# Kernel tuning notes

Hardware: AMD Instinct MI355X
Metric: run time of the kernel (lower is better)

The kernel has to match this reference:

```python
import jax, jax.numpy as jnp
import numpy as np

D = 2048  # dims
T = 8192  # sequence length


def _layernorm(x, g, b):
    m = jnp.mean(x, axis=-1, keepdims=True)
    v = jnp.mean(jnp.square(x - m), axis=-1, keepdims=True)
    return (x - m) * jax.lax.rsqrt(v + 1e-5) * g + b


def _lerp(a, b, t):
    # torch.lerp(a, b, t) = a + t*(b-a)
    return a + t * (b - a)


def _wkv(k, v, time_first, time_decay):
    """RWKV power-decay attention (numerically stable scan).
    k, v: [T, D]. w = -exp(time_decay) is the per-channel log-decay."""
    u = time_first
    w = -jnp.exp(time_decay)

    def step(carry, kv):
        aa, bb, pp = carry  # running num, den, max-exponent, each [D]
        kt, vt = kv
        ww = u + kt
        p = jnp.maximum(pp, ww)
        e1 = jnp.exp(pp - p)
        e2 = jnp.exp(ww - p)
        out = (e1 * aa + e2 * vt) / (e1 * bb + e2)
        ww2 = pp + w
        p2 = jnp.maximum(ww2, kt)
        e1 = jnp.exp(ww2 - p2)
        e2 = jnp.exp(kt - p2)
        return (e1 * aa + e2 * vt, e1 * bb + e2, p2), out

    init = (jnp.zeros((D,), k.dtype), jnp.zeros((D,), k.dtype),
            jnp.full((D,), -1e38, k.dtype))
    _, out = jax.lax.scan(step, init, (k, v))
    return out  # [T, D]


def setup_inputs() -> dict:
    key = jax.random.key(0)
    ks = iter(jax.random.split(key, 40))
    s = 1.0 / np.sqrt(D)
    inp = {"x": jax.random.normal(next(ks), (T, D), jnp.float32)}
    for name in ["attk", "attv", "attr", "atto", "ffnk", "ffnv", "ffnr"]:
        inp[name + "_w"] = jax.random.normal(next(ks), (D, D), jnp.float32) * s
        inp[name + "_b"] = jax.random.normal(next(ks), (D,), jnp.float32) * 0.02
    inp["ln1_g"] = jnp.ones((D,), jnp.float32)
    inp["ln1_b"] = jnp.zeros((D,), jnp.float32)
    inp["ln2_g"] = jnp.ones((D,), jnp.float32)
    inp["ln2_b"] = jnp.zeros((D,), jnp.float32)
    for name in ["attmixk", "attmixv", "attmixr", "ffnmixk", "ffnmixr"]:
        inp[name] = jax.random.uniform(next(ks), (D,), jnp.float32)
    inp["time_first"] = jax.random.normal(next(ks), (D,), jnp.float32) * 0.1
    inp["time_decay"] = jax.random.normal(next(ks), (D,), jnp.float32) * 0.1
    return inp


def reference(x, attk_w, attk_b, attv_w, attv_b, attr_w, attr_b, atto_w, atto_b,
              ffnk_w, ffnk_b, ffnv_w, ffnv_b, ffnr_w, ffnr_b,
              ln1_g, ln1_b, ln2_g, ln2_b,
              attmixk, attmixv, attmixr, ffnmixk, ffnmixr,
              time_first, time_decay):
    # --- time-mix (attention) branch ---
    xy = _layernorm(x, ln1_g, ln1_b)
    tc = jnp.roll(xy, 1, axis=0)  # token shift
    k = _lerp(tc, xy, attmixk) @ attk_w.T + attk_b
    v = _lerp(tc, xy, attmixv) @ attv_w.T + attv_b
    r = jax.nn.sigmoid(_lerp(tc, xy, attmixr) @ attr_w.T + attr_b)
    wkv = _wkv(k, v, time_first, time_decay) * r
    rz = x + wkv @ atto_w.T + atto_b
    # --- channel-mix (FFN) branch ---
    ddd = _layernorm(rz, ln2_g, ln2_b)
    rc = jnp.roll(ddd, 1, axis=0)
    rf = jax.nn.sigmoid(_lerp(rc, ddd, ffnmixr) @ ffnr_w.T + ffnr_b)
    kf = jax.nn.relu(_lerp(rc, ddd, ffnmixk) @ ffnk_w.T + ffnk_b)
    rvm = jnp.square(kf) @ ffnv_w.T + ffnv_b
    return rvm * rf + rz
```

## Files before the change

### kernel.cpp

```cpp
#include <hip/hip_runtime.h>
#include <cstdint>
#include <cstddef>


#define SEQ 8192
#define DIM 2048
#define NCH 128
#define CL  64

typedef unsigned short u16;
typedef __attribute__((ext_vector_type(8))) short bf16x8;
typedef __attribute__((ext_vector_type(4))) float f32x4;

__device__ __forceinline__ u16 f2bf(float f) {
  unsigned x = __float_as_uint(f);
  x += 0x7fffu + ((x >> 16) & 1u);
  return (u16)(x >> 16);
}
__device__ __forceinline__ float bf2f(u16 h) {
  return __uint_as_float((unsigned)h << 16);
}

__global__ void __launch_bounds__(256) convert_weights(
    const float* w0, const float* w1, const float* w2, const float* w3,
    const float* w4, const float* w5, const float* w6, u16* dst)
{
  const float* s;
  switch (blockIdx.y) {
    case 0: s = w0; break; case 1: s = w1; break; case 2: s = w2; break;
    case 3: s = w3; break; case 4: s = w4; break; case 5: s = w5; break;
    default: s = w6; break;
  }
  size_t i = ((size_t)blockIdx.x * 256 + threadIdx.x) * 4;
  float4 f = *(const float4*)(s + i);
  *(ushort4*)(dst + (size_t)blockIdx.y * DIM * DIM + i) =
      make_ushort4(f2bf(f.x), f2bf(f.y), f2bf(f.z), f2bf(f.w));
}

__device__ __forceinline__ void store_mix8(u16* dst, const float* mix,
                                           const float* yc, const float* yp)
{
  float4 ma = *(const float4*)(mix);
  float4 mb = *(const float4*)(mix + 4);
  float mv[8] = {ma.x, ma.y, ma.z, ma.w, mb.x, mb.y, mb.z, mb.w};
  u16 uu[8];
  #pragma unroll
  for (int j = 0; j < 8; ++j)
    uu[j] = f2bf(yp[j] + mv[j] * (yc[j] - yp[j]));
  *(ushort4*)dst       = make_ushort4(uu[0], uu[1], uu[2], uu[3]);
  *(ushort4*)(dst + 4) = make_ushort4(uu[4], uu[5], uu[6], uu[7]);
}

template<int NOUT>
__global__ void __launch_bounds__(256) ln_mix_kernel(
    const float* __restrict__ X, const float* __restrict__ gw, const float* __restrict__ bw,
    const float* __restrict__ mix0, const float* __restrict__ mix1, const float* __restrict__ mix2,
    u16* __restrict__ o0, u16* __restrict__ o1, u16* __restrict__ o2)
{
  const int t  = blockIdx.x;
  const int tp = (t == 0) ? (SEQ - 1) : (t - 1);
  const int tid = threadIdx.x, lane = tid & 63, wid = tid >> 6;
  const int base = tid * 8;
  const float* xc = X + (size_t)t  * DIM + base;
  const float* xp = X + (size_t)tp * DIM + base;
  float4 ca = *(const float4*)xc, cb2 = *(const float4*)(xc + 4);
  float4 pa = *(const float4*)xp, pb2 = *(const float4*)(xp + 4);
  float cv[8] = {ca.x, ca.y, ca.z, ca.w, cb2.x, cb2.y, cb2.z, cb2.w};
  float pv[8] = {pa.x, pa.y, pa.z, pa.w, pb2.x, pb2.y, pb2.z, pb2.w};
  float4 s = {0.f, 0.f, 0.f, 0.f};
  #pragma unroll
  for (int j = 0; j < 8; ++j) {
    s.x += cv[j]; s.y += cv[j] * cv[j];
    s.z += pv[j]; s.w += pv[j] * pv[j];
  }
  #pragma unroll
  for (int off = 32; off > 0; off >>= 1) {
    s.x += __shfl_down(s.x, off);
    s.y += __shfl_down(s.y, off);
    s.z += __shfl_down(s.z, off);
    s.w += __shfl_down(s.w, off);
  }
  __shared__ float4 wred[4];
  if (lane == 0) wred[wid] = s;
  __syncthreads();
  float4 tt;
  tt.x = wred[0].x + wred[1].x + wred[2].x + wred[3].x;
  tt.y = wred[0].y + wred[1].y + wred[2].y + wred[3].y;
  tt.z = wred[0].z + wred[1].z + wred[2].z + wred[3].z;
  tt.w = wred[0].w + wred[1].w + wred[2].w + wred[3].w;
  constexpr float inv = 1.0f / DIM;
  const float mc = tt.x * inv, vc = tt.y * inv - mc * mc;
  const float rc = 1.0f / sqrtf(vc + 1e-5f);
  const float mp = tt.z * inv, vp = tt.w * inv - mp * mp;
  const float rp = 1.0f / sqrtf(vp + 1e-5f);
  float4 ga = *(const float4*)(gw + base), gb = *(const float4*)(gw + base + 4);
  float4 ba = *(const float4*)(bw + base), bb = *(const float4*)(bw + base + 4);
  float gv[8] = {ga.x, ga.y, ga.z, ga.w, gb.x, gb.y, gb.z, gb.w};
  float bv[8] = {ba.x, ba.y, ba.z, ba.w, bb.x, bb.y, bb.z, bb.w};
  float yc[8], yp[8];
  #pragma unroll
  for (int j = 0; j < 8; ++j) {
    yc[j] = (cv[j] - mc) * rc * gv[j] + bv[j];
    yp[j] = (pv[j] - mp) * rp * gv[j] + bv[j];
  }
  store_mix8(o0 + (size_t)t * DIM + base, mix0 + base, yc, yp);
  store_mix8(o1 + (size_t)t * DIM + base, mix1 + base, yc, yp);
  if constexpr (NOUT == 3)
    store_mix8(o2 + (size_t)t * DIM + base, mix2 + base, yc, yp);
}

template<int EPI>
__global__ void __launch_bounds__(512, 2) gemm_bt(
    const u16* __restrict__ A, const u16* __restrict__ B,
    const float* __restrict__ bias,
    const float* __restrict__ exf, const u16* __restrict__ exb,
    float* __restrict__ Cf, u16* __restrict__ Cb)
{
  constexpr int BK = 32;
  constexpr int NT = DIM / BK;
  __shared__ u16 As[4][256 * BK];
  __shared__ u16 Bs[4][256 * BK];
  const int tid  = threadIdx.x;
  const int lane = tid & 63;
  const int wid  = tid >> 6;
  const int wr   = wid >> 2;
  const int wc   = wid & 3;
  const int bid = blockIdx.x;
  const int nb  = (bid & 7) * 32 + (bid >> 3);
  const int tm  = (nb >> 3) * 256;
  const int tn  = (nb & 7) * 256;
  const int frow = lane & 15;
  const int fkc  = lane >> 4;

  f32x4 acc[8][4] = {};

#define STAGE(b, kt)                                                            \
  {                                                                             \
    const int k0 = (kt) * BK;                                                   \
    _Pragma("unroll")                                                           \
    for (int j = 0; j < 2; ++j) {                                               \
      const int p   = (j * 512 + tid) * 16;                                     \
      const int q   = p ^ (((p >> 7) & 3) << 4);                                \
      const int row = q >> 6;                                                   \
      const int ce  = (q & 63) >> 1;                                            \
      __builtin_amdgcn_global_load_lds(                                         \
          (const __attribute__((address_space(1))) void*)                       \
              (A + (size_t)(tm + row) * DIM + k0 + ce),                         \
          (__attribute__((address_space(3))) void*)((char*)&As[b][0] + p),      \
          16, 0, 0);                                                            \
    }                                                                           \
    _Pragma("unroll")                                                           \
    for (int j = 0; j < 2; ++j) {                                               \
      const int p   = (j * 512 + tid) * 16;                                     \
      const int q   = p ^ (((p >> 7) & 3) << 4);                                \
      const int row = q >> 6;                                                   \
      const int ce  = (q & 63) >> 1;                                            \
      __builtin_amdgcn_global_load_lds(                                         \
          (const __attribute__((address_space(1))) void*)                       \
              (B + (size_t)(tn + row) * DIM + k0 + ce),                         \
          (__attribute__((address_space(3))) void*)((char*)&Bs[b][0] + p),      \
          16, 0, 0);                                                            \
    }                                                                           \
  }

#define COMPUTE(b)                                                              \
  {                                                                             \
    bf16x8 af[8], bfr[4];                                                       \
    _Pragma("unroll")                                                           \
    for (int m = 0; m < 8; ++m) {                                               \
      const int row = wr * 128 + m * 16 + frow;                                 \
      const int off = row * 64 + ((fkc ^ ((row >> 1) & 3)) * 16);               \
      af[m] = *(const bf16x8*)((const char*)&As[b][0] + off);                   \
    }                                                                           \
    _Pragma("unroll")                                                           \
    for (int n = 0; n < 4; ++n) {                                               \
      const int row = wc * 64 + n * 16 + frow;                                  \
      const int off = row * 64 + ((fkc ^ ((row >> 1) & 3)) * 16);               \
      bfr[n] = *(const bf16x8*)((const char*)&Bs[b][0] + off);                  \
    }                                                                           \
    __builtin_amdgcn_s_setprio(1);                                              \
    _Pragma("unroll")                                                           \
    for (int m = 0; m < 8; ++m)                                                 \
      _Pragma("unroll")                                                         \
      for (int n = 0; n < 4; ++n)                                               \
        acc[m][n] = __builtin_amdgcn_mfma_f32_16x16x32_bf16(af[m], bfr[n],      \
                                                            acc[m][n], 0, 0, 0);\
    __builtin_amdgcn_s_setprio(0);                                              \
  }

  STAGE(0, 0); STAGE(1, 1); STAGE(2, 2);
  #pragma unroll 1
  for (int t = 0; t < NT - 2; ++t) {
    asm volatile("s_waitcnt vmcnt(8)" ::: "memory");
    __builtin_amdgcn_s_barrier();
    __builtin_amdgcn_sched_barrier(0);
    if (t < NT - 3) STAGE((t + 3) & 3, t + 3);
    COMPUTE(t & 3);
  }
  asm volatile("s_waitcnt vmcnt(4)" ::: "memory");
  __builtin_amdgcn_s_barrier();
  __builtin_amdgcn_sched_barrier(0);
  COMPUTE((NT - 2) & 3);
  asm volatile("s_waitcnt vmcnt(0)" ::: "memory");
  __builtin_amdgcn_s_barrier();
  __builtin_amdgcn_sched_barrier(0);
  COMPUTE((NT - 1) & 3);
#undef STAGE
#undef COMPUTE

  #pragma unroll
  for (int n = 0; n < 4; ++n) {
    const int cn = tn + wc * 64 + n * 16 + frow;
    const float bv = bias[cn];
    #pragma unroll
    for (int m = 0; m < 8; ++m) {
      const int r0 = tm + wr * 128 + m * 16 + (lane >> 4) * 4;
      #pragma unroll
      for (int i = 0; i < 4; ++i) {
        const size_t idx = (size_t)(r0 + i) * DIM + cn;
        float val = acc[m][n][i] + bv;
        if constexpr (EPI == 0)      { Cb[idx] = f2bf(val); }
        else if constexpr (EPI == 1) { Cb[idx] = f2bf(1.0f / (1.0f + __expf(-val))); }
        else if constexpr (EPI == 2) { Cf[idx] = val + exf[idx]; }
        else if constexpr (EPI == 3) { float r = fmaxf(val, 0.0f); Cb[idx] = f2bf(r * r); }
        else                         { Cf[idx] = val * bf2f(exb[idx]) + exf[idx]; }
      }
    }
  }
}

__global__ void __launch_bounds__(256) wkv_phase1(
    const u16* __restrict__ k, const u16* __restrict__ v,
    const float* __restrict__ tdec,
    float* __restrict__ Sa, float* __restrict__ Sb, float* __restrict__ Sp)
{
  const int d = blockIdx.y * 256 + threadIdx.x;
  const int c = blockIdx.x;
  const float w = -__expf(tdec[d]);
  float aa = 0.f, bb = 0.f, pp = -1e38f;
  const int t0 = c * CL;
  for (int t = t0; t < t0 + CL; ++t) {
    const size_t idx = (size_t)t * DIM + d;
    const float kk = bf2f(k[idx]), vv = bf2f(v[idx]);
    const float ww2 = pp + w;
    const float p2 = fmaxf(ww2, kk);
    const float e1 = __expf(ww2 - p2), e2 = __expf(kk - p2);
    aa = e1 * aa + e2 * vv;
    bb = e1 * bb + e2;
    pp = p2;
  }
  Sa[(size_t)c * DIM + d] = aa;
  Sb[(size_t)c * DIM + d] = bb;
  Sp[(size_t)c * DIM + d] = pp;
}

__global__ void __launch_bounds__(256) wkv_phase2(
    const float* __restrict__ Sa, const float* __restrict__ Sb, const float* __restrict__ Sp,
    const float* __restrict__ tdec,
    float* __restrict__ Pa, float* __restrict__ Pb, float* __restrict__ Pp)
{
  const int d = blockIdx.x * 256 + threadIdx.x;
  const float w = -__expf(tdec[d]);
  const float Lw = (float)CL * w;
  float aa = 0.f, bb = 0.f, pp = -1e38f;
  for (int c = 0; c < NCH; ++c) {
    const size_t idx = (size_t)c * DIM + d;
    Pa[idx] = aa; Pb[idx] = bb; Pp[idx] = pp;
    const float dp = pp + Lw;
    const float sa = Sa[idx], sb = Sb[idx], sp = Sp[idx];
    const float p = fmaxf(dp, sp);
    const float e1 = __expf(dp - p), e2 = __expf(sp - p);
    aa = e1 * aa + e2 * sa;
    bb = e1 * bb + e2 * sb;
    pp = p;
  }
}

__global__ void __launch_bounds__(256) wkv_phase3(
    const u16* __restrict__ k, const u16* __restrict__ v, const u16* __restrict__ r,
    const float* __restrict__ Pa, const float* __restrict__ Pb, const float* __restrict__ Pp,
    const float* __restrict__ tfirst, const float* __restrict__ tdec,
    u16* __restrict__ outb)
{
  const int d = blockIdx.y * 256 + threadIdx.x;
  const int c = blockIdx.x;
  const float u = tfirst[d];
  const float w = -__expf(tdec[d]);
  const size_t sidx = (size_t)c * DIM + d;
  float aa = Pa[sidx], bb = Pb[sidx], pp = Pp[sidx];
  const int t0 = c * CL;
  for (int t = t0; t < t0 + CL; ++t) {
    const size_t idx = (size_t)t * DIM + d;
    const float kk = bf2f(k[idx]), vv = bf2f(v[idx]);
    const float ww = u + kk;
    const float p = fmaxf(pp, ww);
    float e1 = __expf(pp - p), e2 = __expf(ww - p);
    const float out = (e1 * aa + e2 * vv) / (e1 * bb + e2);
    outb[idx] = f2bf(out * bf2f(r[idx]));
    const float ww2 = pp + w;
    const float p2 = fmaxf(ww2, kk);
    e1 = __expf(ww2 - p2); e2 = __expf(kk - p2);
    aa = e1 * aa + e2 * vv;
    bb = e1 * bb + e2;
    pp = p2;
  }
}

extern "C" void kernel_launch(void* const* d_in, const int* in_sizes, int n_in,
                              void* d_out, int out_size, void* d_ws, size_t ws_size,
                              hipStream_t stream)
{
  const float* x      = (const float*)d_in[0];
  const float* attk_w = (const float*)d_in[1];
  const float* attk_b = (const float*)d_in[2];
  const float* attv_w = (const float*)d_in[3];
  const float* attv_b = (const float*)d_in[4];
  const float* attr_w = (const float*)d_in[5];
  const float* attr_b = (const float*)d_in[6];
  const float* atto_w = (const float*)d_in[7];
  const float* atto_b = (const float*)d_in[8];
  const float* ffnk_w = (const float*)d_in[9];
  const float* ffnk_b = (const float*)d_in[10];
  const float* ffnv_w = (const float*)d_in[11];
  const float* ffnv_b = (const float*)d_in[12];
  const float* ffnr_w = (const float*)d_in[13];
  const float* ffnr_b = (const float*)d_in[14];
  const float* ln1_g  = (const float*)d_in[15];
  const float* ln1_b  = (const float*)d_in[16];
  const float* ln2_g  = (const float*)d_in[17];
  const float* ln2_b  = (const float*)d_in[18];
  const float* amixk  = (const float*)d_in[19];
  const float* amixv  = (const float*)d_in[20];
  const float* amixr  = (const float*)d_in[21];
  const float* fmixk  = (const float*)d_in[22];
  const float* fmixr  = (const float*)d_in[23];
  const float* tfirst = (const float*)d_in[24];
  const float* tdecay = (const float*)d_in[25];
  float* out = (float*)d_out;

  const size_t WE = (size_t)DIM * DIM;
  const size_t SD = (size_t)SEQ * DIM;
  u16* Wbf = (u16*)d_ws;
  u16* xk  = Wbf + 7 * WE;
  u16* xv  = xk + SD;
  u16* xr  = xv + SD;
  u16* kb  = xr + SD;
  u16* vb  = kb + SD;
  u16* rb  = vb + SD;
  float* Sa = (float*)(rb + SD);
  float* Sb = Sa + (size_t)NCH * DIM;
  float* Sp = Sb + (size_t)NCH * DIM;
  float* Pa = Sp + (size_t)NCH * DIM;
  float* Pb = Pa + (size_t)NCH * DIM;
  float* Pp = Pb + (size_t)NCH * DIM;
  u16*   wkvr = xk;
  float* rz   = (float*)xv;
  u16*   xkf  = kb;
  u16*   xrf  = vb;
  u16*   rf   = rb;
  u16*   kf2  = xk;

  const dim3 gg(256);
  const dim3 gwkv(NCH, DIM / 256);

  convert_weights<<<dim3(DIM * DIM / 1024, 7), 256, 0, stream>>>(
      attk_w, attv_w, attr_w, atto_w, ffnk_w, ffnv_w, ffnr_w, Wbf);

  ln_mix_kernel<3><<<SEQ, 256, 0, stream>>>(x, ln1_g, ln1_b, amixk, amixv, amixr, xk, xv, xr);
  gemm_bt<0><<<gg, 512, 0, stream>>>(xk, Wbf + 0 * WE, attk_b, nullptr, nullptr, nullptr, kb);
  gemm_bt<0><<<gg, 512, 0, stream>>>(xv, Wbf + 1 * WE, attv_b, nullptr, nullptr, nullptr, vb);
  gemm_bt<1><<<gg, 512, 0, stream>>>(xr, Wbf + 2 * WE, attr_b, nullptr, nullptr, nullptr, rb);
  wkv_phase1<<<gwkv, 256, 0, stream>>>(kb, vb, tdecay, Sa, Sb, Sp);
  wkv_phase2<<<DIM / 256, 256, 0, stream>>>(Sa, Sb, Sp, tdecay, Pa, Pb, Pp);
  wkv_phase3<<<gwkv, 256, 0, stream>>>(kb, vb, rb, Pa, Pb, Pp, tfirst, tdecay, wkvr);
  gemm_bt<2><<<gg, 512, 0, stream>>>(wkvr, Wbf + 3 * WE, atto_b, x, nullptr, rz, nullptr);

  ln_mix_kernel<2><<<SEQ, 256, 0, stream>>>(rz, ln2_g, ln2_b, fmixk, fmixr, nullptr, xkf, xrf, nullptr);
  gemm_bt<1><<<gg, 512, 0, stream>>>(xrf, Wbf + 6 * WE, ffnr_b, nullptr, nullptr, nullptr, rf);
  gemm_bt<3><<<gg, 512, 0, stream>>>(xkf, Wbf + 4 * WE, ffnk_b, nullptr, nullptr, nullptr, kf2);
  gemm_bt<4><<<gg, 512, 0, stream>>>(kf2, Wbf + 5 * WE, ffnv_b, rz, rf, out, nullptr);
}
```

Baseline: 1.124 ms.

## Restructure GEMM mainloop into 8-wave ping-pong schedule with BK=64 quadrant stages

Rewrites the bf16 GEMM main loop to use a K tile of 64 with double-buffered LDS split into 128-row halves. Each tile is processed in four sub-blocks (A lo/hi by B lo/hi). Global-to-LDS loads for the next half-tiles are interleaved between these sub-blocks, and barriers and setprio are arranged in a hipBLASLt-style ping-pong. The aim is to overlap LDS reads, global loads and MFMA more finely and to halve the number of K iterations. The cost is many more barriers per iteration, plus the risk that the hand-placed waitcnt accounting races or under-hides latency.

Measured after the change: 1.148 ms. +2.2%, slower.

```diff
diff --git a/kernel.cpp b/kernel.cpp
--- a/kernel.cpp
+++ b/kernel.cpp
@@ -116,10 +116,11 @@
     const float* __restrict__ exf, const u16* __restrict__ exb,
     float* __restrict__ Cf, u16* __restrict__ Cb)
 {
-  constexpr int BK = 32;
-  constexpr int NT = DIM / BK;
-  __shared__ u16 As[4][256 * BK];
-  __shared__ u16 Bs[4][256 * BK];
+  constexpr int BK  = 64;
+  constexpr int NKT = DIM / BK;
+  constexpr int NIT = NKT / 2;
+  __shared__ u16 As[2][2][128 * 64];
+  __shared__ u16 Bs[2][2][128 * 64];
   const int tid  = threadIdx.x;
   const int lane = tid & 63;
   const int wid  = tid >> 6;
@@ -133,80 +134,135 @@
   const int fkc  = lane >> 4;
 
   f32x4 acc[8][4] = {};
-
-#define STAGE(b, kt)                                                            \
-  {                                                                             \
-    const int k0 = (kt) * BK;                                                   \
-    _Pragma("unroll")                                                           \
-    for (int j = 0; j < 2; ++j) {                                               \
-      const int p   = (j * 512 + tid) * 16;                                     \
-      const int q   = p ^ (((p >> 7) & 3) << 4);                                \
-      const int row = q >> 6;                                                   \
-      const int ce  = (q & 63) >> 1;                                            \
-      __builtin_amdgcn_global_load_lds(                                         \
-          (const __attribute__((address_space(1))) void*)                       \
-              (A + (size_t)(tm + row) * DIM + k0 + ce),                         \
-          (__attribute__((address_space(3))) void*)((char*)&As[b][0] + p),      \
-          16, 0, 0);                                                            \
-    }                                                                           \
-    _Pragma("unroll")                                                           \
-    for (int j = 0; j < 2; ++j) {                                               \
-      const int p   = (j * 512 + tid) * 16;                                     \
-      const int q   = p ^ (((p >> 7) & 3) << 4);                                \
-      const int row = q >> 6;                                                   \
-      const int ce  = (q & 63) >> 1;                                            \
-      __builtin_amdgcn_global_load_lds(                                         \
-          (const __attribute__((address_space(1))) void*)                       \
-              (B + (size_t)(tn + row) * DIM + k0 + ce),                         \
-          (__attribute__((address_space(3))) void*)((char*)&Bs[b][0] + p),      \
-          16, 0, 0);                                                            \
-    }                                                                           \
-  }
-
-#define COMPUTE(b)                                                              \
-  {                                                                             \
-    bf16x8 af[8], bfr[4];                                                       \
-    _Pragma("unroll")                                                           \
-    for (int m = 0; m < 8; ++m) {                                               \
-      const int row = wr * 128 + m * 16 + frow;                                 \
-      const int off = row * 64 + ((fkc ^ ((row >> 1) & 3)) * 16);               \
-      af[m] = *(const bf16x8*)((const char*)&As[b][0] + off);                   \
-    }                                                                           \
-    _Pragma("unroll")                                                           \
-    for (int n = 0; n < 4; ++n) {                                               \
-      const int row = wc * 64 + n * 16 + frow;                                  \
-      const int off = row * 64 + ((fkc ^ ((row >> 1) & 3)) * 16);               \
-      bfr[n] = *(const bf16x8*)((const char*)&Bs[b][0] + off);                  \
-    }                                                                           \
-    __builtin_amdgcn_s_setprio(1);                                              \
-    _Pragma("unroll")                                                           \
-    for (int m = 0; m < 8; ++m)                                                 \
-      _Pragma("unroll")                                                         \
-      for (int n = 0; n < 4; ++n)                                               \
-        acc[m][n] = __builtin_amdgcn_mfma_f32_16x16x32_bf16(af[m], bfr[n],      \
-                                                            acc[m][n], 0, 0, 0);\
-    __builtin_amdgcn_s_setprio(0);                                              \
-  }
-
-  STAGE(0, 0); STAGE(1, 1); STAGE(2, 2);
+  bf16x8 aLo[8], aHi[8], bLo[4], bHi[4];
+
+#define BAR  __builtin_amdgcn_s_barrier()
+#define LGK0 { asm volatile("s_waitcnt lgkmcnt(0)" ::: "memory");            \
+               __builtin_amdgcn_sched_barrier(0); }
+#define VMG(N) asm volatile("s_waitcnt vmcnt(" #N ")" ::: "memory")
+
+#define STGA(T, h)                                                            \
+  { _Pragma("unroll")                                                         \
+    for (int j = 0; j < 2; ++j) {                                             \
+      const int p  = (j * 512 + tid) * 16;                                    \
+      const int lr = p >> 7;                                                  \
+      const int cb = (p & 127) ^ ((lr & 7) << 4);                             \
+      __builtin_amdgcn_global_load_lds(                                       \
+        (const __attribute__((address_space(1))) void*)                       \
+            (A + (size_t)(tm + (h) * 128 + lr) * DIM + (T) * BK + (cb >> 1)), \
+        (__attribute__((address_space(3))) void*)((char*)&As[(T)&1][h][0]+p), \
+        16, 0, 0);                                                            \
+    } }
+#define STGB(T, h)                                                            \
+  { _Pragma("unroll")                                                         \
+    for (int j = 0; j < 2; ++j) {                                             \
+      const int p  = (j * 512 + tid) * 16;                                    \
+      const int lr = p >> 7;                                                  \
+      const int cb = (p & 127) ^ ((lr & 7) << 4);                             \
+      __builtin_amdgcn_global_load_lds(                                       \
+        (const __attribute__((address_space(1))) void*)                       \
+            (B + (size_t)(tn + (h) * 128 + lr) * DIM + (T) * BK + (cb >> 1)), \
+        (__attribute__((address_space(3))) void*)((char*)&Bs[(T)&1][h][0]+p), \
+        16, 0, 0);                                                            \
+    } }
+
+#define RDA(dst, db, mm, kk)                                                  \
+  { const int lr_ = (mm) * 16 + frow;                                         \
+    const int cb_ = (kk) * 64 + fkc * 16;                                     \
+    dst = *(const bf16x8*)((const char*)&As[db][wr][0]                        \
+          + lr_ * 128 + (cb_ ^ ((lr_ & 7) << 4))); }
+#define RDB(dst, db, nn, kk)                                                  \
+  { const int lr_ = (wc & 1) * 64 + (nn) * 16 + frow;                         \
+    const int cb_ = (kk) * 64 + fkc * 16;                                     \
+    dst = *(const bf16x8*)((const char*)&Bs[db][wc >> 1][0]                   \
+          + lr_ * 128 + (cb_ ^ ((lr_ & 7) << 4))); }
+
+#define MM(mb, nb_, AF, BF)                                                   \
+  do { __builtin_amdgcn_s_setprio(1);                                         \
+    _Pragma("unroll") for (int m = 0; m < 4; ++m)                             \
+    _Pragma("unroll") for (int n = 0; n < 2; ++n)                             \
+    _Pragma("unroll") for (int ks = 0; ks < 2; ++ks)                          \
+      acc[(mb)+m][(nb_)+n] = __builtin_amdgcn_mfma_f32_16x16x32_bf16(         \
+          (AF)[m*2+ks], (BF)[n*2+ks], acc[(mb)+m][(nb_)+n], 0, 0, 0);         \
+    __builtin_amdgcn_s_setprio(0); } while (0)
+
+#define ITER_BODY(i_, FIRST_, LAST_)                                          \
+  do {                                                                        \
+                                                                     \
+    _Pragma("unroll") for (int m = 0; m < 4; ++m)                             \
+      _Pragma("unroll") for (int ks = 0; ks < 2; ++ks)                        \
+        RDA(aLo[m*2+ks], 0, m, ks);                                           \
+    _Pragma("unroll") for (int n = 0; n < 2; ++n)                             \
+      _Pragma("unroll") for (int ks = 0; ks < 2; ++ks)                        \
+        RDB(bLo[n*2+ks], 0, n, ks);                                           \
+    if (!(FIRST_)) STGA(2*(i_)+1, 0);                                         \
+    BAR; LGK0; MM(0, 0, aLo, bLo); BAR;                                       \
+                                                                     \
+    _Pragma("unroll") for (int n = 0; n < 2; ++n)                             \
+      _Pragma("unroll") for (int ks = 0; ks < 2; ++ks)                        \
+        RDB(bHi[n*2+ks], 0, n + 2, ks);                                       \
+    if (!(FIRST_)) STGA(2*(i_)+1, 1);                                         \
+    BAR; LGK0; MM(0, 2, aLo, bHi); BAR;                                       \
+                                                                     \
+    _Pragma("unroll") for (int m = 0; m < 4; ++m)                             \
+      _Pragma("unroll") for (int ks = 0; ks < 2; ++ks)                        \
+        RDA(aHi[m*2+ks], 0, m + 4, ks);                                       \
+    if (!(LAST_)) STGB(2*(i_)+2, 0);                                          \
+    BAR; LGK0; MM(4, 0, aHi, bLo); BAR;                                       \
+                                               \
+    if (!(LAST_)) STGB(2*(i_)+2, 1);                                          \
+    BAR; MM(4, 2, aHi, bHi);                                                  \
+    if (LAST_) { VMG(0); } else { VMG(4); }                                   \
+    __builtin_amdgcn_sched_barrier(0);                                        \
+    BAR;                                                                      \
+                                                                     \
+    _Pragma("unroll") for (int m = 0; m < 4; ++m)                             \
+      _Pragma("unroll") for (int ks = 0; ks < 2; ++ks)                        \
+        RDA(aLo[m*2+ks], 1, m, ks);                                           \
+    _Pragma("unroll") for (int n = 0; n < 2; ++n)                             \
+      _Pragma("unroll") for (int ks = 0; ks < 2; ++ks)                        \
+        RDB(bLo[n*2+ks], 1, n, ks);                                           \
+    if (!(LAST_)) STGA(2*(i_)+2, 0);                                          \
+    BAR; LGK0; MM(0, 0, aLo, bLo); BAR;                                       \
+                                                                     \
+    _Pragma("unroll") for (int n = 0; n < 2; ++n)                             \
+      _Pragma("unroll") for (int ks = 0; ks < 2; ++ks)                        \
+        RDB(bHi[n*2+ks], 1, n + 2, ks);                                       \
+    if (!(LAST_)) STGA(2*(i_)+2, 1);                                          \
+    BAR; LGK0; MM(0, 2, aLo, bHi); BAR;                                       \
+                                                                     \
+    _Pragma("unroll") for (int m = 0; m < 4; ++m)                             \
+      _Pragma("unroll") for (int ks = 0; ks < 2; ++ks)                        \
+        RDA(aHi[m*2+ks], 1, m + 4, ks);                                       \
+    if (!(LAST_)) STGB(2*(i_)+3, 0);                                          \
+    BAR; LGK0; MM(4, 0, aHi, bLo); BAR;                                       \
+                                          \
+    if (!(LAST_)) STGB(2*(i_)+3, 1);                                          \
+    BAR; MM(4, 2, aHi, bHi);                                                  \
+    if (!(LAST_)) { VMG(4); __builtin_amdgcn_sched_barrier(0); }              \
+    BAR;                                                                      \
+  } while (0)
+
+  STGA(0, 0); STGA(0, 1); STGB(0, 0); STGB(0, 1);
+  STGA(1, 0); STGA(1, 1); STGB(1, 0); STGB(1, 1);
+  VMG(0);
+  __builtin_amdgcn_sched_barrier(0);
+  BAR;
+
+  ITER_BODY(0, true, false);
   #pragma unroll 1
-  for (int t = 0; t < NT - 2; ++t) {
-    asm volatile("s_waitcnt vmcnt(8)" ::: "memory");
-    __builtin_amdgcn_s_barrier();
-    __builtin_amdgcn_sched_barrier(0);
-    if (t < NT - 3) STAGE((t + 3) & 3, t + 3);
-    COMPUTE(t & 3);
-  }
-  asm volatile("s_waitcnt vmcnt(4)" ::: "memory");
-  __builtin_amdgcn_s_barrier();
-  __builtin_amdgcn_sched_barrier(0);
-  COMPUTE((NT - 2) & 3);
-  asm volatile("s_waitcnt vmcnt(0)" ::: "memory");
-  __builtin_amdgcn_s_barrier();
-  __builtin_amdgcn_sched_barrier(0);
-  COMPUTE((NT - 1) & 3);
-#undef STAGE
-#undef COMPUTE
+  for (int i = 1; i < NIT - 1; ++i) ITER_BODY(i, false, false);
+  ITER_BODY(NIT - 1, false, true);
+
+#undef ITER_BODY
+#undef MM
+#undef RDA
+#undef RDB
+#undef STGA
+#undef STGB
+#undef VMG
+#undef LGK0
+#undef BAR
 
   #pragma unroll
   for (int n = 0; n < 4; ++n) {
```
